# Kernel tuning notes

Hardware: AMD Instinct MI355X
Metric: run time of the kernel (lower is better)

## Reference

```python
import jax, jax.numpy as jnp
import numpy as np

D_MODEL = 768
N_HEADS = 4
N_POINTS = 4
PATCH = 16
IMG = 224
HF = IMG // PATCH  # 14
WF = IMG // PATCH  # 14
LQ = HF * WF       # 196 tokens
DH = D_MODEL // N_HEADS  # 192


def setup_inputs() -> dict:
    key = jax.random.key(0)
    ks = jax.random.split(key, 14)
    s = 0.02
    inp = {
        "x": jax.random.normal(ks[0], (4, 16, 3, IMG, IMG), dtype=jnp.float32),
        # patch-embed conv (Conv2d 3->768, k=16, s=16)
        "embed_w": s * jax.random.normal(ks[1], (D_MODEL, 3, PATCH, PATCH), dtype=jnp.float32),
        "embed_b": jnp.zeros((D_MODEL,), dtype=jnp.float32),
        # MSDeformAttn linears (nn.Linear stores W as [out, in]; y = x @ W.T + b)
        "value_w": s * jax.random.normal(ks[2], (D_MODEL, D_MODEL), dtype=jnp.float32),
        "value_b": jnp.zeros((D_MODEL,), dtype=jnp.float32),
        "off_w": s * jax.random.normal(ks[3], (N_HEADS * N_POINTS * 2, D_MODEL), dtype=jnp.float32),
        "off_b": s * jax.random.normal(ks[4], (N_HEADS * N_POINTS * 2,), dtype=jnp.float32),
        "aw_w": s * jax.random.normal(ks[5], (N_HEADS * N_POINTS, D_MODEL), dtype=jnp.float32),
        "aw_b": jnp.zeros((N_HEADS * N_POINTS,), dtype=jnp.float32),
        "outp_w": s * jax.random.normal(ks[6], (D_MODEL, D_MODEL), dtype=jnp.float32),
        "outp_b": jnp.zeros((D_MODEL,), dtype=jnp.float32),
        # final nn.Linear proj
        "proj_w": s * jax.random.normal(ks[7], (D_MODEL, D_MODEL), dtype=jnp.float32),
        "proj_b": jnp.zeros((D_MODEL,), dtype=jnp.float32),
    }
    return inp


def _patch_embed(x, w, b):
    # x: (N,3,H,W); non-overlapping 16x16 patches == Conv2d(3,D,16,16)
    N = x.shape[0]
    xh = x.reshape(N, 3, HF, PATCH, WF, PATCH)
    feat = jnp.einsum('nchpwq,dcpq->nhwd', xh, w) + b  # (N,HF,WF,D)
    return feat.reshape(N, LQ, D_MODEL)


def _ref_points():
    lin = jnp.linspace(0.0, 1.0, HF)
    gy, gx = jnp.meshgrid(lin, lin, indexing='ij')
    return jnp.stack([gx, gy], -1).reshape(LQ, 2)  # (Lq, 2) in [0,1], (x,y)


def _deform_attn_core(value, loc, attn):
    # value: (N, Lq, M, Dh); loc: (N, Lq, M, P, 2) normalized [0,1]; attn: (N, Lq, M, P)
    N = value.shape[0]
    # grid_sample align_corners=False: pixel = (2*loc-1 + 1)*S/2 - 0.5 = loc*S - 0.5
    px = loc[..., 0] * WF - 0.5
    py = loc[..., 1] * HF - 0.5
    x0 = jnp.floor(px).astype(jnp.int32)
    y0 = jnp.floor(py).astype(jnp.int32)
    x1, y1 = x0 + 1, y0 + 1
    wx1 = px - x0.astype(px.dtype)
    wy1 = py - y0.astype(py.dtype)
    wx0, wy0 = 1.0 - wx1, 1.0 - wy1

    valh = value.transpose(0, 2, 1, 3)  # (N, M, HW, Dh)

    def gather(ix, iy):
        valid = (ix >= 0) & (ix < WF) & (iy >= 0) & (iy < HF)  # zeros padding
        idx = jnp.clip(iy, 0, HF - 1) * WF + jnp.clip(ix, 0, WF - 1)
        idxm = idx.transpose(0, 2, 1, 3).reshape(N, N_HEADS, LQ * N_POINTS)
        g = jnp.take_along_axis(valh, idxm[..., None], axis=2)  # (N,M,Lq*P,Dh)
        g = g * valid.transpose(0, 2, 1, 3).reshape(N, N_HEADS, LQ * N_POINTS, 1)
        return g.reshape(N, N_HEADS, LQ, N_POINTS, DH)

    def w4(a, b):  # (N,Lq,M,P) -> (N,M,Lq,P,1)
        return (a * b).transpose(0, 2, 1, 3)[..., None]

    sampled = (w4(wx0, wy0) * gather(x0, y0) + w4(wx1, wy0) * gather(x1, y0)
               + w4(wx0, wy1) * gather(x0, y1) + w4(wx1, wy1) * gather(x1, y1))
    # weighted combine over points
    out = (sampled * attn.transpose(0, 2, 1, 3)[..., None]).sum(3)  # (N,M,Lq,Dh)
    return out.transpose(0, 2, 1, 3).reshape(N, LQ, D_MODEL)


def reference(x, embed_w, embed_b, value_w, value_b, off_w, off_b, aw_w, aw_b,
              outp_w, outp_b, proj_w, proj_b):
    B, T = x.shape[0], x.shape[1]
    N = B * T
    xi = x.reshape(N, 3, IMG, IMG)
    feat = _patch_embed(xi, embed_w, embed_b)  # (N, Lq, D)

    # MSDeformAttn (n_levels=1)
    value = (feat @ value_w.T + value_b).reshape(N, LQ, N_HEADS, DH)
    off = (feat @ off_w.T + off_b).reshape(N, LQ, N_HEADS, N_POINTS, 2)
    aw = (feat @ aw_w.T + aw_b).reshape(N, LQ, N_HEADS, N_POINTS)
    aw = jax.nn.softmax(aw, axis=-1)  # softmax over n_levels*n_points = 4

    ref = _ref_points()  # (Lq, 2)
    norm = jnp.array([WF, HF], dtype=feat.dtype)  # offset_normalizer = (W, H)
    loc = ref[None, :, None, None, :] + off / norm  # (N,Lq,M,P,2)

    out = _deform_attn_core(value, loc, aw)
    out = out @ outp_w.T + outp_b  # output_proj

    pooled = out.mean(axis=1)  # mean over tokens
    final = pooled @ proj_w.T + proj_b
    return final.reshape(B, T, D_MODEL)
```

## Files before the change

kernel.cpp:

```cpp
#include <hip/hip_runtime.h>
#include <hip/hip_bf16.h>


using bf16 = __bf16;
typedef bf16  bf16x8 __attribute__((ext_vector_type(8)));
typedef float f32x4  __attribute__((ext_vector_type(4)));

#define N_IMG   64
#define LQ      196
#define DM      768
#define NH      4
#define DH      192
#define M_ROWS  (N_IMG * LQ)
#define NCAT    896

#define OFF_A      ((size_t)0)
#define OFF_WEMBT  (OFF_A     + 19267584)
#define OFF_WCAT   (OFF_WEMBT + 1179648)
#define OFF_WFUSE  (OFF_WCAT  + 1376256)
#define OFF_BFUSE  (OFF_WFUSE + 1376256)
#define OFF_ZB     (OFF_BFUSE + 4096)
#define OFF_OA     (OFF_ZB    + 4096)
#define OFF_CORE   (OFF_OA    + 3211264)
#define OFF_POOL   (OFF_CORE  + 196608)

__device__ __forceinline__ void gload_lds16(const bf16* g, bf16* l) {
#if __has_builtin(__builtin_amdgcn_global_load_lds)
  __builtin_amdgcn_global_load_lds(
      (const __attribute__((address_space(1))) void*)g,
      (__attribute__((address_space(3))) void*)l, 16, 0, 0);
#else
  *(bf16x8*)l = *(const bf16x8*)g;
#endif
}

__global__ void stage_kernel(const float* __restrict__ x,
                             const float* __restrict__ embed_w,
                             const float* __restrict__ embed_b,
                             const float* __restrict__ value_w,
                             const float* __restrict__ off_w,
                             const float* __restrict__ aw_w,
                             const float* __restrict__ value_b,
                             const float* __restrict__ off_b,
                             const float* __restrict__ aw_b,
                             bf16* __restrict__ A,
                             bf16* __restrict__ WembT, bf16* __restrict__ Wcat,
                             float* __restrict__ bfused, float* __restrict__ zb) {
  const int bid = blockIdx.x;
  if (bid < 9408) {
    const int t   = bid * 256 + threadIdx.x;
    const int row = t / 192;
    const int j   = t - row * 192;
    const int k   = j * 4;
    const int c   = k >> 8;
    const int r   = k & 255;
    const int p   = r >> 4;
    const int q   = r & 15;
    const int n   = row / 196;
    const int lq  = row - n * 196;
    const int h   = lq / 14;
    const int w   = lq - h * 14;
    const float4 v = *(const float4*)(x +
        ((((size_t)n * 3 + c) * 224) + h * 16 + p) * 224 + w * 16 + q);
    bf16* dst = A + (size_t)row * DM + k;
    dst[0] = (bf16)v.x; dst[1] = (bf16)v.y; dst[2] = (bf16)v.z; dst[3] = (bf16)v.w;
    return;
  }
  if (bid < 12096) {
    const int idx = (bid - 9408) * 256 + threadIdx.x;
    {
      int rr = idx / DM, kk = idx - rr * DM;
      float v = 0.f;
      if (rr < 768)       v = value_w[idx];
      else if (rr < 800)  v = off_w[(rr - 768) * DM + kk];
      else if (rr < 816)  v = aw_w[(rr - 800) * DM + kk];
      Wcat[idx] = (bf16)v;
    }
    if (idx < DM * DM) {
      int kk = idx / DM, jj = idx - kk * DM;
      WembT[idx] = (bf16)embed_w[(size_t)jj * DM + kk];
    }
    if (idx < DM) zb[idx] = 0.f;
    return;
  }
  const int t  = threadIdx.x;
  const int r  = (bid - 12096) * 32 + (t >> 3);
  const int t8 = t & 7;
  const float* src = nullptr;
  float badd = 0.f;
  if (r < 768)      { src = value_w + (size_t)r * DM;        badd = value_b[r]; }
  else if (r < 800) { src = off_w  + (size_t)(r - 768) * DM; badd = off_b[r - 768]; }
  else if (r < 816) { src = aw_w   + (size_t)(r - 800) * DM; badd = aw_b[r - 800]; }
  float s = 0.f;
  if (src) {
    for (int j = t8; j < DM; j += 8) s += src[j] * embed_b[j];
  }
#pragma unroll
  for (int o = 4; o >= 1; o >>= 1) s += __shfl_down(s, o, 8);
  if (t8 == 0) bfused[r] = (src ? s + badd : 0.f);
}

__global__ void gemm_bt(const bf16* __restrict__ A, const bf16* __restrict__ B,
                        const float* __restrict__ bias, bf16* __restrict__ C,
                        int M, int N, int K) {
  __shared__ bf16 As[128 * 64];
  __shared__ bf16 Bs[128 * 64];

  const int tid  = threadIdx.x;
  const int wave = tid >> 6;
  const int lane = tid & 63;
  const int nBase = blockIdx.x * 128;
  const int mBase = blockIdx.y * 128;
  const int wm = wave & 1;
  const int wn = wave >> 1;
  const int quad = lane >> 4;
  const int r16  = lane & 15;

  const f32x4 zero = {0.f, 0.f, 0.f, 0.f};
  f32x4 acc[4][4];
#pragma unroll
  for (int mi = 0; mi < 4; ++mi)
#pragma unroll
    for (int ni = 0; ni < 4; ++ni) acc[mi][ni] = zero;

  const int srow = wave * 32 + (lane >> 3);
  const int scol = (lane & 7) * 8;
  const bf16* Ag = A + (size_t)(mBase + srow) * K + scol;
  const bf16* Bg = B + (size_t)(nBase + srow) * K + scol;
  bf16* Al = As + srow * 64 + scol;
  bf16* Bl = Bs + srow * 64 + scol;

  for (int kt = 0; kt < K; kt += 64) {
#pragma unroll
    for (int i = 0; i < 4; ++i) {
      gload_lds16(Ag + (size_t)(i * 8) * K + kt, Al + i * 8 * 64);
      gload_lds16(Bg + (size_t)(i * 8) * K + kt, Bl + i * 8 * 64);
    }
    __syncthreads();
#pragma unroll
    for (int kk = 0; kk < 64; kk += 32) {
      bf16x8 af[4], bfr[4];
#pragma unroll
      for (int mi = 0; mi < 4; ++mi)
        af[mi] = *(const bf16x8*)&As[(wm * 64 + mi * 16 + r16) * 64 + kk + quad * 8];
#pragma unroll
      for (int ni = 0; ni < 4; ++ni)
        bfr[ni] = *(const bf16x8*)&Bs[(wn * 64 + ni * 16 + r16) * 64 + kk + quad * 8];
#pragma unroll
      for (int mi = 0; mi < 4; ++mi)
#pragma unroll
        for (int ni = 0; ni < 4; ++ni)
          acc[mi][ni] = __builtin_amdgcn_mfma_f32_16x16x32_bf16(
              af[mi], bfr[ni], acc[mi][ni], 0, 0, 0);
    }
    __syncthreads();
  }

#pragma unroll
  for (int ni = 0; ni < 4; ++ni) {
    const int col = nBase + wn * 64 + ni * 16 + r16;
    const float bv = bias[col];
#pragma unroll
    for (int mi = 0; mi < 4; ++mi) {
      const int row0 = mBase + wm * 64 + mi * 16 + quad * 4;
#pragma unroll
      for (int rr = 0; rr < 4; ++rr) {
        C[(size_t)(row0 + rr) * N + col] = (bf16)(acc[mi][ni][rr] + bv);
      }
    }
  }
}

__global__ void gemm_oa(const bf16* __restrict__ A, const bf16* __restrict__ B,
                        const float* __restrict__ bias, float* __restrict__ OA,
                        int K) {
  __shared__ bf16 As[128 * 64];
  __shared__ bf16 Bs[128 * 64];

  const int tid  = threadIdx.x;
  const int wave = tid >> 6;
  const int lane = tid & 63;
  const int mBase = blockIdx.x * 128;
  const int wm = wave & 1;
  const int wn = wave >> 1;
  const int quad = lane >> 4;
  const int r16  = lane & 15;

  const f32x4 zero = {0.f, 0.f, 0.f, 0.f};
  f32x4 acc[4][4];
#pragma unroll
  for (int mi = 0; mi < 4; ++mi)
#pragma unroll
    for (int ni = 0; ni < 4; ++ni) acc[mi][ni] = zero;

  const int srow = wave * 32 + (lane >> 3);
  const int scol = (lane & 7) * 8;
  const bf16* Ag = A + (size_t)(mBase + srow) * K + scol;
  const bf16* Bg = B + (size_t)srow * K + scol;
  bf16* Al = As + srow * 64 + scol;
  bf16* Bl = Bs + srow * 64 + scol;

  for (int kt = 0; kt < K; kt += 64) {
#pragma unroll
    for (int i = 0; i < 4; ++i) {
      gload_lds16(Ag + (size_t)(i * 8) * K + kt, Al + i * 8 * 64);
      gload_lds16(Bg + (size_t)(i * 8) * K + kt, Bl + i * 8 * 64);
    }
    __syncthreads();
#pragma unroll
    for (int kk = 0; kk < 64; kk += 32) {
      bf16x8 af[4], bfr[4];
#pragma unroll
      for (int mi = 0; mi < 4; ++mi)
        af[mi] = *(const bf16x8*)&As[(wm * 64 + mi * 16 + r16) * 64 + kk + quad * 8];
#pragma unroll
      for (int ni = 0; ni < 4; ++ni)
        bfr[ni] = *(const bf16x8*)&Bs[(wn * 64 + ni * 16 + r16) * 64 + kk + quad * 8];
#pragma unroll
      for (int mi = 0; mi < 4; ++mi)
#pragma unroll
        for (int ni = 0; ni < 4; ++ni)
          acc[mi][ni] = __builtin_amdgcn_mfma_f32_16x16x32_bf16(
              af[mi], bfr[ni], acc[mi][ni], 0, 0, 0);
    }
    __syncthreads();
  }

#pragma unroll
  for (int ni = 0; ni < 4; ++ni) {
    const int col = wn * 64 + ni * 16 + r16;
    if (col >= 64) continue;
    const float bv = bias[col];
#pragma unroll
    for (int mi = 0; mi < 4; ++mi) {
      const int row0 = mBase + wm * 64 + mi * 16 + quad * 4;
#pragma unroll
      for (int rr = 0; rr < 4; ++rr) {
        OA[(size_t)(row0 + rr) * 64 + col] = acc[mi][ni][rr] + bv;
      }
    }
  }
}

__global__ void percore_kernel(const bf16* __restrict__ A,
                               const float* __restrict__ OA,
                               const bf16* __restrict__ Wfused,
                               const float* __restrict__ bfused,
                               float* __restrict__ core) {
  __shared__ float sC[LQ];
  __shared__ float sP[4][DM];
  __shared__ float sS[DM];
  __shared__ float sSum;

  const int n = blockIdx.x;
  const int m = blockIdx.y;
  const int tid = threadIdx.x;

  if (tid < LQ) sC[tid] = 0.f;
  if (tid == 0) sSum = 0.f;
  __syncthreads();

  const float* oa = OA + (size_t)n * LQ * 64;
  for (int t = tid; t < LQ * 4; t += 256) {
    const int lq = t >> 2, p = t & 3;
    const float* row = oa + (size_t)lq * 64;
    const float l0 = row[32 + m * 4 + 0];
    const float l1 = row[32 + m * 4 + 1];
    const float l2 = row[32 + m * 4 + 2];
    const float l3 = row[32 + m * 4 + 3];
    const float mx = fmaxf(fmaxf(l0, l1), fmaxf(l2, l3));
    const float e0 = __expf(l0 - mx), e1 = __expf(l1 - mx);
    const float e2 = __expf(l2 - mx), e3 = __expf(l3 - mx);
    const float inv = 1.f / (e0 + e1 + e2 + e3);
    const float ep[4] = {e0, e1, e2, e3};
    const float ew = ep[p] * inv;

    const int h = lq / 14, w = lq - (lq / 14) * 14;
    const float px = (float)w * (14.f / 13.f) - 0.5f + row[(m * 4 + p) * 2 + 0];
    const float py = (float)h * (14.f / 13.f) - 0.5f + row[(m * 4 + p) * 2 + 1];
    const float fx = floorf(px), fy = floorf(py);
    const int x0 = (int)fx, y0 = (int)fy;
    const float wx1 = px - fx, wy1 = py - fy;
    const float wx0 = 1.f - wx1, wy0 = 1.f - wy1;

    const bool vx0 = (x0 >= 0) & (x0 < 14);
    const bool vx1 = (x0 >= -1) & (x0 < 13);
    const bool vy0 = (y0 >= 0) & (y0 < 14);
    const bool vy1 = (y0 >= -1) & (y0 < 13);
    const int cx0 = min(max(x0, 0), 13),      cx1 = min(max(x0 + 1, 0), 13);
    const int cy0 = min(max(y0, 0), 13) * 14, cy1 = min(max(y0 + 1, 0), 13) * 14;

    atomicAdd(&sC[cy0 + cx0], (vx0 & vy0) ? ew * wx0 * wy0 : 0.f);
    atomicAdd(&sC[cy0 + cx1], (vx1 & vy0) ? ew * wx1 * wy0 : 0.f);
    atomicAdd(&sC[cy1 + cx0], (vx0 & vy1) ? ew * wx0 * wy1 : 0.f);
    atomicAdd(&sC[cy1 + cx1], (vx1 & vy1) ? ew * wx1 * wy1 : 0.f);
  }
  __syncthreads();
  if (tid < LQ) atomicAdd(&sSum, sC[tid]);

  {
    const int q = tid >> 6, lane = tid & 63;
    const bf16* an = A + (size_t)n * LQ * DM;
    float acc[12];
#pragma unroll
    for (int j = 0; j < 12; ++j) acc[j] = 0.f;
    const int t0 = q * 49;
    for (int tok = t0; tok < t0 + 49; ++tok) {
      const float cf = sC[tok];
      const bf16* ar = an + (size_t)tok * DM + lane;
#pragma unroll
      for (int j = 0; j < 12; ++j) acc[j] += cf * (float)ar[64 * j];
    }
#pragma unroll
    for (int j = 0; j < 12; ++j) sP[q][lane + 64 * j] = acc[j];
  }
  __syncthreads();
  for (int c = tid; c < DM; c += 256)
    sS[c] = sP[0][c] + sP[1][c] + sP[2][c] + sP[3][c];
  __syncthreads();

  if (tid < DH) {
    const int ch = m * DH + tid;
    const bf16* wr = Wfused + (size_t)ch * DM;
    float acc = 0.f;
    for (int k = 0; k < DM; k += 8) {
      const bf16x8 wv = *(const bf16x8*)(wr + k);
#pragma unroll
      for (int j = 0; j < 8; ++j) acc += (float)wv[j] * sS[k + j];
    }
    core[(size_t)n * DM + ch] = (acc + sSum * bfused[ch]) * (1.f / 196.f);
  }
}

__global__ void small_linear(const float* __restrict__ in,
                             const float* __restrict__ W,
                             const float* __restrict__ b,
                             float* __restrict__ out) {
  const int n = blockIdx.x;
  const int d = blockIdx.y * 256 + threadIdx.x;
  const float4* a4 = (const float4*)(in + (size_t)n * DM);
  const float4* w4 = (const float4*)(W + (size_t)d * DM);
  float acc = 0.f;
#pragma unroll 4
  for (int k = 0; k < DM / 4; ++k) {
    float4 a = a4[k], w = w4[k];
    acc += a.x * w.x + a.y * w.y + a.z * w.z + a.w * w.w;
  }
  out[(size_t)n * DM + d] = acc + b[d];
}

extern "C" void kernel_launch(void* const* d_in, const int* in_sizes, int n_in,
                              void* d_out, int out_size, void* d_ws, size_t ws_size,
                              hipStream_t stream) {
  const float* x       = (const float*)d_in[0];
  const float* embed_w = (const float*)d_in[1];
  const float* embed_b = (const float*)d_in[2];
  const float* value_w = (const float*)d_in[3];
  const float* value_b = (const float*)d_in[4];
  const float* off_w   = (const float*)d_in[5];
  const float* off_b   = (const float*)d_in[6];
  const float* aw_w    = (const float*)d_in[7];
  const float* aw_b    = (const float*)d_in[8];
  const float* outp_w  = (const float*)d_in[9];
  const float* outp_b  = (const float*)d_in[10];
  const float* proj_w  = (const float*)d_in[11];
  const float* proj_b  = (const float*)d_in[12];
  float* out = (float*)d_out;

  char* ws = (char*)d_ws;
  bf16*  A      = (bf16*)(ws + OFF_A);
  bf16*  WembT  = (bf16*)(ws + OFF_WEMBT);
  bf16*  Wcat   = (bf16*)(ws + OFF_WCAT);
  bf16*  Wfused = (bf16*)(ws + OFF_WFUSE);
  float* bfused = (float*)(ws + OFF_BFUSE);
  float* zb     = (float*)(ws + OFF_ZB);
  float* OA     = (float*)(ws + OFF_OA);
  float* core   = (float*)(ws + OFF_CORE);
  float* pooled = (float*)(ws + OFF_POOL);

  stage_kernel<<<dim3(12124), dim3(256), 0, stream>>>(
      x, embed_w, embed_b, value_w, off_w, aw_w, value_b, off_b, aw_b,
      A, WembT, Wcat, bfused, zb);

  gemm_bt<<<dim3(DM / 128, NCAT / 128), dim3(256), 0, stream>>>(
      Wcat, WembT, zb, Wfused, NCAT, DM, DM);

  gemm_oa<<<dim3(M_ROWS / 128), dim3(256), 0, stream>>>(
      A, Wfused + (size_t)768 * DM, bfused + 768, OA, DM);

  percore_kernel<<<dim3(N_IMG, NH), dim3(256), 0, stream>>>(
      A, OA, Wfused, bfused, core);

  small_linear<<<dim3(64, 3), dim3(256), 0, stream>>>(core, outp_w, outp_b, pooled);
  small_linear<<<dim3(64, 3), dim3(256), 0, stream>>>(pooled, proj_w, proj_b, out);
}
```

Before: 248.6 us.

## Fold weight products into stage kernel and pre-fuse output and final projections

Removes the separate bf16 MFMA GEMM that formed Wcat·embed_wᵀ. The fused value/offset/attention weight is now computed directly in fp32 inside the staging kernel with scalar FMAs, and bf16 staging copies of the weights are no longer written. The output projection and the final proj are also pre-multiplied into a single matrix Wpp and bias bpp, so the tail needs one small linear launch instead of two. The cost is about 600 blocks each doing a 768-long serial dot-product loop over uncoalesced weight reads, plus an extra 768³ fp32 product done on CUDA cores every call. This could lengthen the staging kernel's critical path.

```diff
diff --git a/kernel.cpp b/kernel.cpp
--- a/kernel.cpp
+++ b/kernel.cpp
@@ -12,17 +12,14 @@
 #define NH      4
 #define DH      192
 #define M_ROWS  (N_IMG * LQ)
-#define NCAT    896
 
 #define OFF_A      ((size_t)0)
-#define OFF_WEMBT  (OFF_A     + 19267584)
-#define OFF_WCAT   (OFF_WEMBT + 1179648)
-#define OFF_WFUSE  (OFF_WCAT  + 1376256)
+#define OFF_WFUSE  (OFF_A     + 19267584)
 #define OFF_BFUSE  (OFF_WFUSE + 1376256)
-#define OFF_ZB     (OFF_BFUSE + 4096)
-#define OFF_OA     (OFF_ZB    + 4096)
+#define OFF_WPP    (OFF_BFUSE + 4096)
+#define OFF_BPP    (OFF_WPP   + 2359296)
+#define OFF_OA     (OFF_BPP   + 4096)
 #define OFF_CORE   (OFF_OA    + 3211264)
-#define OFF_POOL   (OFF_CORE  + 196608)
 
 __device__ __forceinline__ void gload_lds16(const bf16* g, bf16* l) {
 #if __has_builtin(__builtin_amdgcn_global_load_lds)
@@ -43,132 +40,110 @@
                              const float* __restrict__ value_b,
                              const float* __restrict__ off_b,
                              const float* __restrict__ aw_b,
+                             const float* __restrict__ outp_w,
+                             const float* __restrict__ outp_b,
+                             const float* __restrict__ proj_w,
+                             const float* __restrict__ proj_b,
                              bf16* __restrict__ A,
-                             bf16* __restrict__ WembT, bf16* __restrict__ Wcat,
-                             float* __restrict__ bfused, float* __restrict__ zb) {
+                             bf16* __restrict__ Wfused,
+                             float* __restrict__ bfused,
+                             float* __restrict__ Wpp,
+                             float* __restrict__ bpp) {
   const int bid = blockIdx.x;
-  if (bid < 9408) {
-    const int t   = bid * 256 + threadIdx.x;
-    const int row = t / 192;
-    const int j   = t - row * 192;
-    const int k   = j * 4;
-    const int c   = k >> 8;
-    const int r   = k & 255;
-    const int p   = r >> 4;
-    const int q   = r & 15;
-    const int n   = row / 196;
-    const int lq  = row - n * 196;
-    const int h   = lq / 14;
-    const int w   = lq - h * 14;
-    const float4 v = *(const float4*)(x +
-        ((((size_t)n * 3 + c) * 224) + h * 16 + p) * 224 + w * 16 + q);
-    bf16* dst = A + (size_t)row * DM + k;
-    dst[0] = (bf16)v.x; dst[1] = (bf16)v.y; dst[2] = (bf16)v.z; dst[3] = (bf16)v.w;
+  const int tid = threadIdx.x;
+
+  if (bid < 306) {
+    const int rt = bid / 6, kt = bid - rt * 6;
+    const int r0 = rt * 16;
+    const int k  = kt * 128 + (tid & 127);
+    const int rh = tid >> 7;
+    const float* src;
+    if (rt < 48)      src = value_w + (size_t)(r0 + rh * 8) * DM;
+    else if (rt < 50) src = off_w  + (size_t)(r0 - 768 + rh * 8) * DM;
+    else              src = aw_w   + (size_t)(r0 - 800 + rh * 8) * DM;
+    float acc[8];
+#pragma unroll
+    for (int i = 0; i < 8; ++i) acc[i] = 0.f;
+#pragma unroll 4
+    for (int j = 0; j < DM; ++j) {
+      const float e = embed_w[(size_t)j * DM + k];
+#pragma unroll
+      for (int i = 0; i < 8; ++i) acc[i] += src[(size_t)i * DM + j] * e;
+    }
+#pragma unroll
+    for (int i = 0; i < 8; ++i)
+      Wfused[(size_t)(r0 + rh * 8 + i) * DM + k] = (bf16)acc[i];
     return;
   }
-  if (bid < 12096) {
-    const int idx = (bid - 9408) * 256 + threadIdx.x;
-    {
-      int rr = idx / DM, kk = idx - rr * DM;
-      float v = 0.f;
-      if (rr < 768)       v = value_w[idx];
-      else if (rr < 800)  v = off_w[(rr - 768) * DM + kk];
-      else if (rr < 816)  v = aw_w[(rr - 800) * DM + kk];
-      Wcat[idx] = (bf16)v;
-    }
-    if (idx < DM * DM) {
-      int kk = idx / DM, jj = idx - kk * DM;
-      WembT[idx] = (bf16)embed_w[(size_t)jj * DM + kk];
-    }
-    if (idx < DM) zb[idx] = 0.f;
+  if (bid < 594) {
+    const int b  = bid - 306;
+    const int rt = b / 6, kt = b - rt * 6;
+    const int r0 = rt * 16;
+    const int k  = kt * 128 + (tid & 127);
+    const int rh = tid >> 7;
+    const float* src = proj_w + (size_t)(r0 + rh * 8) * DM;
+    float acc[8];
+#pragma unroll
+    for (int i = 0; i < 8; ++i) acc[i] = 0.f;
+#pragma unroll 4
+    for (int j = 0; j < DM; ++j) {
+      const float e = outp_w[(size_t)j * DM + k];
+#pragma unroll
+      for (int i = 0; i < 8; ++i) acc[i] += src[(size_t)i * DM + j] * e;
+    }
+#pragma unroll
+    for (int i = 0; i < 8; ++i)
+      Wpp[(size_t)(r0 + rh * 8 + i) * DM + k] = acc[i];
     return;
   }
-  const int t  = threadIdx.x;
-  const int r  = (bid - 12096) * 32 + (t >> 3);
-  const int t8 = t & 7;
-  const float* src = nullptr;
-  float badd = 0.f;
-  if (r < 768)      { src = value_w + (size_t)r * DM;        badd = value_b[r]; }
-  else if (r < 800) { src = off_w  + (size_t)(r - 768) * DM; badd = off_b[r - 768]; }
-  else if (r < 816) { src = aw_w   + (size_t)(r - 800) * DM; badd = aw_b[r - 800]; }
-  float s = 0.f;
-  if (src) {
-    for (int j = t8; j < DM; j += 8) s += src[j] * embed_b[j];
-  }
-#pragma unroll
-  for (int o = 4; o >= 1; o >>= 1) s += __shfl_down(s, o, 8);
-  if (t8 == 0) bfused[r] = (src ? s + badd : 0.f);
-}
-
-__global__ void gemm_bt(const bf16* __restrict__ A, const bf16* __restrict__ B,
-                        const float* __restrict__ bias, bf16* __restrict__ C,
-                        int M, int N, int K) {
-  __shared__ bf16 As[128 * 64];
-  __shared__ bf16 Bs[128 * 64];
-
-  const int tid  = threadIdx.x;
-  const int wave = tid >> 6;
-  const int lane = tid & 63;
-  const int nBase = blockIdx.x * 128;
-  const int mBase = blockIdx.y * 128;
-  const int wm = wave & 1;
-  const int wn = wave >> 1;
-  const int quad = lane >> 4;
-  const int r16  = lane & 15;
-
-  const f32x4 zero = {0.f, 0.f, 0.f, 0.f};
-  f32x4 acc[4][4];
-#pragma unroll
-  for (int mi = 0; mi < 4; ++mi)
-#pragma unroll
-    for (int ni = 0; ni < 4; ++ni) acc[mi][ni] = zero;
-
-  const int srow = wave * 32 + (lane >> 3);
-  const int scol = (lane & 7) * 8;
-  const bf16* Ag = A + (size_t)(mBase + srow) * K + scol;
-  const bf16* Bg = B + (size_t)(nBase + srow) * K + scol;
-  bf16* Al = As + srow * 64 + scol;
-  bf16* Bl = Bs + srow * 64 + scol;
-
-  for (int kt = 0; kt < K; kt += 64) {
-#pragma unroll
-    for (int i = 0; i < 4; ++i) {
-      gload_lds16(Ag + (size_t)(i * 8) * K + kt, Al + i * 8 * 64);
-      gload_lds16(Bg + (size_t)(i * 8) * K + kt, Bl + i * 8 * 64);
-    }
-    __syncthreads();
-#pragma unroll
-    for (int kk = 0; kk < 64; kk += 32) {
-      bf16x8 af[4], bfr[4];
-#pragma unroll
-      for (int mi = 0; mi < 4; ++mi)
-        af[mi] = *(const bf16x8*)&As[(wm * 64 + mi * 16 + r16) * 64 + kk + quad * 8];
-#pragma unroll
-      for (int ni = 0; ni < 4; ++ni)
-        bfr[ni] = *(const bf16x8*)&Bs[(wn * 64 + ni * 16 + r16) * 64 + kk + quad * 8];
-#pragma unroll
-      for (int mi = 0; mi < 4; ++mi)
-#pragma unroll
-        for (int ni = 0; ni < 4; ++ni)
-          acc[mi][ni] = __builtin_amdgcn_mfma_f32_16x16x32_bf16(
-              af[mi], bfr[ni], acc[mi][ni], 0, 0, 0);
-    }
-    __syncthreads();
-  }
-
-#pragma unroll
-  for (int ni = 0; ni < 4; ++ni) {
-    const int col = nBase + wn * 64 + ni * 16 + r16;
-    const float bv = bias[col];
-#pragma unroll
-    for (int mi = 0; mi < 4; ++mi) {
-      const int row0 = mBase + wm * 64 + mi * 16 + quad * 4;
-#pragma unroll
-      for (int rr = 0; rr < 4; ++rr) {
-        C[(size_t)(row0 + rr) * N + col] = (bf16)(acc[mi][ni][rr] + bv);
-      }
-    }
-  }
+  if (bid < 661) {
+    const int mb = bid - 594;
+    if (mb < 28) {
+      const int r  = mb * 32 + (tid >> 3);
+      const int t8 = tid & 7;
+      const float* src = nullptr;
+      float badd = 0.f;
+      if (r < 768)      { src = value_w + (size_t)r * DM;        badd = value_b[r]; }
+      else if (r < 800) { src = off_w  + (size_t)(r - 768) * DM; badd = off_b[r - 768]; }
+      else if (r < 816) { src = aw_w   + (size_t)(r - 800) * DM; badd = aw_b[r - 800]; }
+      float s = 0.f;
+      if (src) for (int j = t8; j < DM; j += 8) s += src[j] * embed_b[j];
+#pragma unroll
+      for (int o = 4; o >= 1; o >>= 1) s += __shfl_down(s, o, 8);
+      if (t8 == 0) bfused[r] = (src ? s + badd : 0.f);
+    } else if (mb < 52) {
+      const int r  = (mb - 28) * 32 + (tid >> 3);
+      const int t8 = tid & 7;
+      const float* src = proj_w + (size_t)r * DM;
+      float s = 0.f;
+      for (int j = t8; j < DM; j += 8) s += src[j] * outp_b[j];
+#pragma unroll
+      for (int o = 4; o >= 1; o >>= 1) s += __shfl_down(s, o, 8);
+      if (t8 == 0) bpp[r] = s + proj_b[r];
+    } else {
+      const int idx = (mb - 52) * 4096 + tid * 16;
+      bf16* dst = Wfused + (size_t)816 * DM + idx;
+#pragma unroll
+      for (int i = 0; i < 16; ++i) dst[i] = (bf16)0.f;
+    }
+    return;
+  }
+  const int t   = (bid - 661) * 256 + tid;
+  const int row = t / 192;
+  const int j   = t - row * 192;
+  const int k   = j * 4;
+  const int c   = k >> 8;
+  const int r   = k & 255;
+  const int p   = r >> 4;
+  const int q   = r & 15;
+  const int n   = row / 196;
+  const int lq  = row - n * 196;
+  const int h   = lq / 14;
+  const int w   = lq - h * 14;
+  const float4 v = *(const float4*)(x +
+      ((((size_t)n * 3 + c) * 224) + h * 16 + p) * 224 + w * 16 + q);
+  bf16* dst = A + (size_t)row * DM + k;
+  dst[0] = (bf16)v.x; dst[1] = (bf16)v.y; dst[2] = (bf16)v.z; dst[3] = (bf16)v.w;
 }
 
 __global__ void gemm_oa(const bf16* __restrict__ A, const bf16* __restrict__ B,
@@ -332,7 +307,7 @@
   }
 }
 
-__global__ void small_linear(const float* __restrict__ in,
+__global__ void final_linear(const float* __restrict__ in,
                              const float* __restrict__ W,
                              const float* __restrict__ b,
                              float* __restrict__ out) {
@@ -369,21 +344,16 @@
 
   char* ws = (char*)d_ws;
   bf16*  A      = (bf16*)(ws + OFF_A);
-  bf16*  WembT  = (bf16*)(ws + OFF_WEMBT);
-  bf16*  Wcat   = (bf16*)(ws + OFF_WCAT);
   bf16*  Wfused = (bf16*)(ws + OFF_WFUSE);
   float* bfused = (float*)(ws + OFF_BFUSE);
-  float* zb     = (float*)(ws + OFF_ZB);
+  float* Wpp    = (float*)(ws + OFF_WPP);
+  float* bpp    = (float*)(ws + OFF_BPP);
   float* OA     = (float*)(ws + OFF_OA);
   float* core   = (float*)(ws + OFF_CORE);
-  float* pooled = (float*)(ws + OFF_POOL);
-
-  stage_kernel<<<dim3(12124), dim3(256), 0, stream>>>(
+
+  stage_kernel<<<dim3(10069), dim3(256), 0, stream>>>(
       x, embed_w, embed_b, value_w, off_w, aw_w, value_b, off_b, aw_b,
-      A, WembT, Wcat, bfused, zb);
-
-  gemm_bt<<<dim3(DM / 128, NCAT / 128), dim3(256), 0, stream>>>(
-      Wcat, WembT, zb, Wfused, NCAT, DM, DM);
+      outp_w, outp_b, proj_w, proj_b, A, Wfused, bfused, Wpp, bpp);
 
   gemm_oa<<<dim3(M_ROWS / 128), dim3(256), 0, stream>>>(
       A, Wfused + (size_t)768 * DM, bfused + 768, OA, DM);
@@ -391,6 +361,5 @@
   percore_kernel<<<dim3(N_IMG, NH), dim3(256), 0, stream>>>(
       A, OA, Wfused, bfused, core);
 
-  small_linear<<<dim3(64, 3), dim3(256), 0, stream>>>(core, outp_w, outp_b, pooled);
-  small_linear<<<dim3(64, 3), dim3(256), 0, stream>>>(pooled, proj_w, proj_b, out);
-}
+  final_linear<<<dim3(64, 3), dim3(256), 0, stream>>>(core, Wpp, bpp, out);
+}
```

Result: slower. 319.9 us (+28.7%).

## Fuse weight-fold GEMM into staging kernel, converting fp32 weights on the fly

Applied to the files above, without the earlier changes.

Folds the Wcat×WembT weight-fusion GEMM into the staging kernel. The first 42 blocks read the fp32 value/off/aw weights and the embed weights directly, convert them to bf16 while staging them into shared memory, and transpose the embed weights in the same step. This removes the separate Wcat/WembT bf16 staging buffers, the zero-bias buffer, and one kernel launch with its global round trip. The cost is fp32 global reads and scattered two-byte LDS stores for the transpose. Those 42 GEMM blocks also run alongside the patch-copy blocks, and the longest of them may set the kernel's tail latency.

```diff
diff --git a/kernel.cpp b/kernel.cpp
--- a/kernel.cpp
+++ b/kernel.cpp
@@ -3,6 +3,7 @@
 
 
 using bf16 = __bf16;
+typedef bf16  bf16x4 __attribute__((ext_vector_type(4)));
 typedef bf16  bf16x8 __attribute__((ext_vector_type(8)));
 typedef float f32x4  __attribute__((ext_vector_type(4)));
 
@@ -12,15 +13,11 @@
 #define NH      4
 #define DH      192
 #define M_ROWS  (N_IMG * LQ)
-#define NCAT    896
 
 #define OFF_A      ((size_t)0)
-#define OFF_WEMBT  (OFF_A     + 19267584)
-#define OFF_WCAT   (OFF_WEMBT + 1179648)
-#define OFF_WFUSE  (OFF_WCAT  + 1376256)
+#define OFF_WFUSE  (OFF_A     + 19267584)
 #define OFF_BFUSE  (OFF_WFUSE + 1376256)
-#define OFF_ZB     (OFF_BFUSE + 4096)
-#define OFF_OA     (OFF_ZB    + 4096)
+#define OFF_OA     (OFF_BFUSE + 4096)
 #define OFF_CORE   (OFF_OA    + 3211264)
 #define OFF_POOL   (OFF_CORE  + 196608)
 
@@ -44,131 +41,117 @@
                              const float* __restrict__ off_b,
                              const float* __restrict__ aw_b,
                              bf16* __restrict__ A,
-                             bf16* __restrict__ WembT, bf16* __restrict__ Wcat,
-                             float* __restrict__ bfused, float* __restrict__ zb) {
-  const int bid = blockIdx.x;
-  if (bid < 9408) {
-    const int t   = bid * 256 + threadIdx.x;
-    const int row = t / 192;
-    const int j   = t - row * 192;
-    const int k   = j * 4;
-    const int c   = k >> 8;
-    const int r   = k & 255;
-    const int p   = r >> 4;
-    const int q   = r & 15;
-    const int n   = row / 196;
-    const int lq  = row - n * 196;
-    const int h   = lq / 14;
-    const int w   = lq - h * 14;
-    const float4 v = *(const float4*)(x +
-        ((((size_t)n * 3 + c) * 224) + h * 16 + p) * 224 + w * 16 + q);
-    bf16* dst = A + (size_t)row * DM + k;
-    dst[0] = (bf16)v.x; dst[1] = (bf16)v.y; dst[2] = (bf16)v.z; dst[3] = (bf16)v.w;
-    return;
-  }
-  if (bid < 12096) {
-    const int idx = (bid - 9408) * 256 + threadIdx.x;
-    {
-      int rr = idx / DM, kk = idx - rr * DM;
-      float v = 0.f;
-      if (rr < 768)       v = value_w[idx];
-      else if (rr < 800)  v = off_w[(rr - 768) * DM + kk];
-      else if (rr < 816)  v = aw_w[(rr - 800) * DM + kk];
-      Wcat[idx] = (bf16)v;
-    }
-    if (idx < DM * DM) {
-      int kk = idx / DM, jj = idx - kk * DM;
-      WembT[idx] = (bf16)embed_w[(size_t)jj * DM + kk];
-    }
-    if (idx < DM) zb[idx] = 0.f;
-    return;
-  }
-  const int t  = threadIdx.x;
-  const int r  = (bid - 12096) * 32 + (t >> 3);
-  const int t8 = t & 7;
-  const float* src = nullptr;
-  float badd = 0.f;
-  if (r < 768)      { src = value_w + (size_t)r * DM;        badd = value_b[r]; }
-  else if (r < 800) { src = off_w  + (size_t)(r - 768) * DM; badd = off_b[r - 768]; }
-  else if (r < 816) { src = aw_w   + (size_t)(r - 800) * DM; badd = aw_b[r - 800]; }
-  float s = 0.f;
-  if (src) {
-    for (int j = t8; j < DM; j += 8) s += src[j] * embed_b[j];
-  }
-#pragma unroll
-  for (int o = 4; o >= 1; o >>= 1) s += __shfl_down(s, o, 8);
-  if (t8 == 0) bfused[r] = (src ? s + badd : 0.f);
-}
-
-__global__ void gemm_bt(const bf16* __restrict__ A, const bf16* __restrict__ B,
-                        const float* __restrict__ bias, bf16* __restrict__ C,
-                        int M, int N, int K) {
+                             bf16* __restrict__ Wfused,
+                             float* __restrict__ bfused) {
   __shared__ bf16 As[128 * 64];
   __shared__ bf16 Bs[128 * 64];
 
-  const int tid  = threadIdx.x;
-  const int wave = tid >> 6;
-  const int lane = tid & 63;
-  const int nBase = blockIdx.x * 128;
-  const int mBase = blockIdx.y * 128;
-  const int wm = wave & 1;
-  const int wn = wave >> 1;
-  const int quad = lane >> 4;
-  const int r16  = lane & 15;
-
-  const f32x4 zero = {0.f, 0.f, 0.f, 0.f};
-  f32x4 acc[4][4];
-#pragma unroll
-  for (int mi = 0; mi < 4; ++mi)
-#pragma unroll
-    for (int ni = 0; ni < 4; ++ni) acc[mi][ni] = zero;
-
-  const int srow = wave * 32 + (lane >> 3);
-  const int scol = (lane & 7) * 8;
-  const bf16* Ag = A + (size_t)(mBase + srow) * K + scol;
-  const bf16* Bg = B + (size_t)(nBase + srow) * K + scol;
-  bf16* Al = As + srow * 64 + scol;
-  bf16* Bl = Bs + srow * 64 + scol;
-
-  for (int kt = 0; kt < K; kt += 64) {
-#pragma unroll
-    for (int i = 0; i < 4; ++i) {
-      gload_lds16(Ag + (size_t)(i * 8) * K + kt, Al + i * 8 * 64);
-      gload_lds16(Bg + (size_t)(i * 8) * K + kt, Bl + i * 8 * 64);
-    }
-    __syncthreads();
-#pragma unroll
-    for (int kk = 0; kk < 64; kk += 32) {
-      bf16x8 af[4], bfr[4];
-#pragma unroll
-      for (int mi = 0; mi < 4; ++mi)
-        af[mi] = *(const bf16x8*)&As[(wm * 64 + mi * 16 + r16) * 64 + kk + quad * 8];
-#pragma unroll
-      for (int ni = 0; ni < 4; ++ni)
-        bfr[ni] = *(const bf16x8*)&Bs[(wn * 64 + ni * 16 + r16) * 64 + kk + quad * 8];
-#pragma unroll
-      for (int mi = 0; mi < 4; ++mi)
+  const int bid = blockIdx.x;
+  const int tid = threadIdx.x;
+
+  if (bid < 42) {
+    const int rt = bid / 6, kt = bid - rt * 6;
+    const int r0 = rt * 128, k0 = kt * 128;
+    const int wave = tid >> 6;
+    const int lane = tid & 63;
+    const int wm = wave & 1, wn = wave >> 1;
+    const int quad = lane >> 4, r16 = lane & 15;
+
+    const f32x4 zero = {0.f, 0.f, 0.f, 0.f};
+    f32x4 acc[4][4];
+#pragma unroll
+    for (int mi = 0; mi < 4; ++mi)
+#pragma unroll
+      for (int ni = 0; ni < 4; ++ni) acc[mi][ni] = zero;
+
+    for (int jt = 0; jt < DM; jt += 64) {
+#pragma unroll
+      for (int p = 0; p < 8; ++p) {
+        const int i   = p * 256 + tid;
+        const int row = i >> 4;
+        const int c4  = (i & 15) * 4;
+        const int r   = r0 + row;
+        float4 v = {0.f, 0.f, 0.f, 0.f};
+        if (r < 768)      v = *(const float4*)(value_w + (size_t)r * DM + jt + c4);
+        else if (r < 800) v = *(const float4*)(off_w + (size_t)(r - 768) * DM + jt + c4);
+        else if (r < 816) v = *(const float4*)(aw_w  + (size_t)(r - 800) * DM + jt + c4);
+        bf16x4 b4 = {(bf16)v.x, (bf16)v.y, (bf16)v.z, (bf16)v.w};
+        *(bf16x4*)&As[row * 64 + c4] = b4;
+      }
+#pragma unroll
+      for (int p = 0; p < 8; ++p) {
+        const int i  = p * 256 + tid;
+        const int j  = i & 63;
+        const int kq = i >> 6;
+        const float4 v = *(const float4*)(embed_w + (size_t)(jt + j) * DM + k0 + kq * 4);
+        Bs[(kq * 4 + 0) * 64 + j] = (bf16)v.x;
+        Bs[(kq * 4 + 1) * 64 + j] = (bf16)v.y;
+        Bs[(kq * 4 + 2) * 64 + j] = (bf16)v.z;
+        Bs[(kq * 4 + 3) * 64 + j] = (bf16)v.w;
+      }
+      __syncthreads();
+#pragma unroll
+      for (int kk = 0; kk < 64; kk += 32) {
+        bf16x8 af[4], bfr[4];
+#pragma unroll
+        for (int mi = 0; mi < 4; ++mi)
+          af[mi] = *(const bf16x8*)&As[(wm * 64 + mi * 16 + r16) * 64 + kk + quad * 8];
 #pragma unroll
         for (int ni = 0; ni < 4; ++ni)
-          acc[mi][ni] = __builtin_amdgcn_mfma_f32_16x16x32_bf16(
-              af[mi], bfr[ni], acc[mi][ni], 0, 0, 0);
-    }
-    __syncthreads();
-  }
-
-#pragma unroll
-  for (int ni = 0; ni < 4; ++ni) {
-    const int col = nBase + wn * 64 + ni * 16 + r16;
-    const float bv = bias[col];
-#pragma unroll
-    for (int mi = 0; mi < 4; ++mi) {
-      const int row0 = mBase + wm * 64 + mi * 16 + quad * 4;
-#pragma unroll
-      for (int rr = 0; rr < 4; ++rr) {
-        C[(size_t)(row0 + rr) * N + col] = (bf16)(acc[mi][ni][rr] + bv);
-      }
-    }
-  }
+          bfr[ni] = *(const bf16x8*)&Bs[(wn * 64 + ni * 16 + r16) * 64 + kk + quad * 8];
+#pragma unroll
+        for (int mi = 0; mi < 4; ++mi)
+#pragma unroll
+          for (int ni = 0; ni < 4; ++ni)
+            acc[mi][ni] = __builtin_amdgcn_mfma_f32_16x16x32_bf16(
+                af[mi], bfr[ni], acc[mi][ni], 0, 0, 0);
+      }
+      __syncthreads();
+    }
+#pragma unroll
+    for (int ni = 0; ni < 4; ++ni) {
+      const int col = k0 + wn * 64 + ni * 16 + r16;
+#pragma unroll
+      for (int mi = 0; mi < 4; ++mi) {
+        const int row0 = r0 + wm * 64 + mi * 16 + quad * 4;
+#pragma unroll
+        for (int rr = 0; rr < 4; ++rr)
+          Wfused[(size_t)(row0 + rr) * DM + col] = (bf16)acc[mi][ni][rr];
+      }
+    }
+    return;
+  }
+  if (bid < 70) {
+    const int r  = (bid - 42) * 32 + (tid >> 3);
+    const int t8 = tid & 7;
+    const float* src = nullptr;
+    float badd = 0.f;
+    if (r < 768)      { src = value_w + (size_t)r * DM;        badd = value_b[r]; }
+    else if (r < 800) { src = off_w  + (size_t)(r - 768) * DM; badd = off_b[r - 768]; }
+    else if (r < 816) { src = aw_w   + (size_t)(r - 800) * DM; badd = aw_b[r - 800]; }
+    float s = 0.f;
+    if (src) for (int j = t8; j < DM; j += 8) s += src[j] * embed_b[j];
+#pragma unroll
+    for (int o = 4; o >= 1; o >>= 1) s += __shfl_down(s, o, 8);
+    if (t8 == 0) bfused[r] = (src ? s + badd : 0.f);
+    return;
+  }
+  const int t   = (bid - 70) * 256 + tid;
+  const int row = t / 192;
+  const int j   = t - row * 192;
+  const int k   = j * 4;
+  const int c   = k >> 8;
+  const int r   = k & 255;
+  const int p   = r >> 4;
+  const int q   = r & 15;
+  const int n   = row / 196;
+  const int lq  = row - n * 196;
+  const int h   = lq / 14;
+  const int w   = lq - h * 14;
+  const float4 v = *(const float4*)(x +
+      ((((size_t)n * 3 + c) * 224) + h * 16 + p) * 224 + w * 16 + q);
+  bf16* dst = A + (size_t)row * DM + k;
+  dst[0] = (bf16)v.x; dst[1] = (bf16)v.y; dst[2] = (bf16)v.z; dst[3] = (bf16)v.w;
 }
 
 __global__ void gemm_oa(const bf16* __restrict__ A, const bf16* __restrict__ B,
@@ -369,21 +352,15 @@
 
   char* ws = (char*)d_ws;
   bf16*  A      = (bf16*)(ws + OFF_A);
-  bf16*  WembT  = (bf16*)(ws + OFF_WEMBT);
-  bf16*  Wcat   = (bf16*)(ws + OFF_WCAT);
   bf16*  Wfused = (bf16*)(ws + OFF_WFUSE);
   float* bfused = (float*)(ws + OFF_BFUSE);
-  float* zb     = (float*)(ws + OFF_ZB);
   float* OA     = (float*)(ws + OFF_OA);
   float* core   = (float*)(ws + OFF_CORE);
   float* pooled = (float*)(ws + OFF_POOL);
 
-  stage_kernel<<<dim3(12124), dim3(256), 0, stream>>>(
+  stage_kernel<<<dim3(9478), dim3(256), 0, stream>>>(
       x, embed_w, embed_b, value_w, off_w, aw_w, value_b, off_b, aw_b,
-      A, WembT, Wcat, bfused, zb);
-
-  gemm_bt<<<dim3(DM / 128, NCAT / 128), dim3(256), 0, stream>>>(
-      Wcat, WembT, zb, Wfused, NCAT, DM, DM);
+      A, Wfused, bfused);
 
   gemm_oa<<<dim3(M_ROWS / 128), dim3(256), 0, stream>>>(
       A, Wfused + (size_t)768 * DM, bfused + 768, OA, DM);
```

Result: slower. 319.0 us (+28.3%).
